# Kernel tuning notes

Hardware: AMD Instinct MI355X
Metric: run time of the kernel (lower is better)

## Reference

```python
import jax, jax.numpy as jnp
import numpy as np

N = 50000      # nodes
E = 800000     # edges (avg degree 16)
EMB = 128      # emb_dim
NF = 7         # x_features
EF = 5         # edge_features
L = 5          # num_layer
BN_EPS = 1e-5


def setup_inputs() -> dict:
    key = jax.random.key(0)
    ks = jax.random.split(key, 12)
    s = 0.05
    return {
        "x": jax.random.normal(ks[0], (N, NF), jnp.float32),
        "edge_attr": jax.random.normal(ks[1], (E, EF), jnp.float32),
        "edge_index": jax.random.randint(ks[2], (2, E), 0, N, dtype=jnp.int32),
        "W_x": jax.random.normal(ks[3], (NF, EMB), jnp.float32) * s,
        "b_x": jax.random.normal(ks[4], (NF, EMB), jnp.float32) * s,
        "W_e": jax.random.normal(ks[5], (L, EF, EMB), jnp.float32) * s,
        "b_e": jax.random.normal(ks[6], (L, EF, EMB), jnp.float32) * s,
        # per-layer GIN update MLP: Linear(EMB,2EMB)-ReLU-Linear(2EMB,EMB)
        "W1": jax.random.normal(ks[7], (L, EMB, 2 * EMB), jnp.float32) * s,
        "b1": jnp.zeros((L, 2 * EMB), jnp.float32),
        "W2": jax.random.normal(ks[8], (L, 2 * EMB, EMB), jnp.float32) * s,
        "b2": jnp.zeros((L, EMB), jnp.float32),
        # per-layer BatchNorm1d affine params
        "gamma": jnp.ones((L, EMB), jnp.float32),
        "beta": jnp.zeros((L, EMB), jnp.float32),
    }


def reference(x, edge_attr, W_x, b_x, W_e, b_e, W1, b1, W2, b2, gamma, beta, edge_index):
    src, dst = edge_index[0], edge_index[1]
    # initial node embedding: sum of 7 Linear(1,EMB) applied per column == x @ W_x + sum(biases)
    h = x @ W_x + b_x.sum(axis=0)  # [N, EMB]
    for l in range(L):
        # edge embeddings: sum of EF Linear(1,EMB) over edge_attr columns
        e_emb = edge_attr @ W_e[l] + b_e[l].sum(axis=0)  # [E, EMB]
        sl_emb = b_e[l].sum(axis=0)  # self-loop edges have zero attr -> bias sum
        # message = x_j + edge_emb, aggr = add (scatter over dst); self loops add h + sl_emb
        msg = h[src] + e_emb                                        # [E, EMB]
        agg = jax.ops.segment_sum(msg, dst, num_segments=N) + h + sl_emb  # [N, EMB]
        # GIN update MLP
        z = jax.nn.relu(agg @ W1[l] + b1[l]) @ W2[l] + b2[l]        # [N, EMB]
        # BatchNorm1d (training-mode batch stats, biased variance)
        mu = z.mean(axis=0)
        var = z.var(axis=0)
        z = (z - mu) * jax.lax.rsqrt(var + BN_EPS) * gamma[l] + beta[l]
        # ELU on all but last layer; dropout is identity at drop_ratio=0; JK='last'
        h = jax.nn.elu(z) if l < L - 1 else z
    return h
```

## Files before the change

### kernel.cpp

```cpp
#include <hip/hip_runtime.h>
#include <math.h>

#define NN 50000
#define NE 800000
#define EMB 128
#define HID 256
#define NF 7
#define EF 5
#define NL 5
#define BN_EPS 1e-5f
#define NREP 32
#define SCAN_B 196
#define NBUCK 49

typedef _Float16 f16x8 __attribute__((ext_vector_type(8)));
typedef _Float16 f16x2 __attribute__((ext_vector_type(2)));
typedef __attribute__((ext_vector_type(4))) float f32x4;

__device__ inline unsigned pkh2(float a, float b) {
    union { unsigned v; _Float16 h[2]; } x;
    x.h[0] = (_Float16)a; x.h[1] = (_Float16)b;
    return x.v;
}
__device__ inline float2 uph2(unsigned u) {
    union { unsigned v; _Float16 h[2]; } x; x.v = u;
    return make_float2((float)x.h[0], (float)x.h[1]);
}
__device__ inline unsigned short f2h_bits(float f) {
    _Float16 h = (_Float16)f;
    return __builtin_bit_cast(unsigned short, h);
}
__device__ inline float h_bits2f(unsigned short b) {
    return (float)__builtin_bit_cast(_Float16, b);
}
__device__ inline f16x2 as_h2(unsigned u) { return __builtin_bit_cast(f16x2, u); }

__global__ void k_prep(const float* __restrict__ b_x, const float* __restrict__ b_e,
                       float* __restrict__ bsum_x, float* __restrict__ bsum_e,
                       int* __restrict__ counts, int* __restrict__ cursor,
                       float* __restrict__ stats) {
    int tid = threadIdx.x;
    if (blockIdx.x == 0 && tid < EMB) {
        float s = 0.f;
        for (int f = 0; f < NF; ++f) s += b_x[f * EMB + tid];
        bsum_x[tid] = s;
        for (int l = 0; l < NL; ++l) {
            float se = 0.f;
            for (int f = 0; f < EF; ++f) se += b_e[(l * EF + f) * EMB + tid];
            bsum_e[l * EMB + tid] = se;
        }
    }
    int gid = blockIdx.x * blockDim.x + tid;
    int stride = gridDim.x * blockDim.x;
    for (int i = gid; i < NN; i += stride) { counts[i] = 0; cursor[i] = 0; }
    const int STOT = NL * NREP * 2 * EMB;
    for (int i = gid; i < STOT; i += stride) stats[i] = 0.f;
}

__global__ void k_prepw(const float* __restrict__ W1, const float* __restrict__ W2,
                        unsigned short* __restrict__ W1ph, unsigned short* __restrict__ W1pl,
                        unsigned short* __restrict__ W2ph, unsigned short* __restrict__ W2pl) {
    const int TOT = NL * EMB * HID;
    int gid = blockIdx.x * blockDim.x + threadIdx.x;
    if (gid < TOT) {
        int l = gid / (EMB * HID);
        int r = gid % (EMB * HID);
        int w = r >> 13;
        int rem = r & 8191;
        int h2 = rem >> 11;
        int rem2 = rem & 2047;
        int kk = rem2 >> 9;
        int rem3 = rem2 & 511;
        int lane = rem3 >> 3;
        int j = rem3 & 7;
        int hc = w * 64 + h2 * 16 + (lane & 15);
        int k = kk * 32 + (lane >> 4) * 8 + j;
        float wv = W1[((size_t)l * EMB + k) * HID + hc];
        unsigned short hi = f2h_bits(wv);
        W1ph[gid] = hi;
        W1pl[gid] = f2h_bits(wv - h_bits2f(hi));
    } else if (gid < 2 * TOT) {
        int g = gid - TOT;
        int l = g / (EMB * HID);
        int r = g % (EMB * HID);
        int w = r >> 13;
        int rem = r & 8191;
        int o2 = rem >> 12;
        int rem2 = rem & 4095;
        int kk = rem2 >> 9;
        int rem3 = rem2 & 511;
        int lane = rem3 >> 3;
        int j = rem3 & 7;
        int oc = w * 32 + o2 * 16 + (lane & 15);
        int k2 = kk * 32 + (lane >> 4) * 8 + j;
        float wv = W2[((size_t)l * HID + k2) * EMB + oc];
        unsigned short hi = f2h_bits(wv);
        W2ph[g] = hi;
        W2pl[g] = f2h_bits(wv - h_bits2f(hi));
    }
}

__global__ void k_init(const float* __restrict__ x, const float* __restrict__ W_x,
                       const float* __restrict__ bsum_x, unsigned short* __restrict__ h16) {
    int gid = blockIdx.x * blockDim.x + threadIdx.x;
    int v = gid >> 5;
    if (v >= NN) return;
    int c = (gid & 31) << 2;
    float4 acc = *(const float4*)(bsum_x + c);
    #pragma unroll
    for (int f = 0; f < NF; ++f) {
        float xv = x[(size_t)v * NF + f];
        float4 w = *(const float4*)(W_x + f * EMB + c);
        acc.x += xv * w.x; acc.y += xv * w.y; acc.z += xv * w.z; acc.w += xv * w.w;
    }
    uint2 p = make_uint2(pkh2(acc.x, acc.y), pkh2(acc.z, acc.w));
    *(uint2*)(h16 + (size_t)v * EMB + c) = p;
}

__global__ void k_hist(const int* __restrict__ dst, int* __restrict__ counts) {
    int e = blockIdx.x * blockDim.x + threadIdx.x;
    if (e < NE) atomicAdd(&counts[dst[e]], 1);
}

__global__ void k_scan1(const int* __restrict__ counts, int* __restrict__ bsum) {
    int tid = threadIdx.x;
    int i = blockIdx.x * 256 + tid;
    int v = (i < NN) ? counts[i] : 0;
    #pragma unroll
    for (int off = 1; off < 64; off <<= 1) v += __shfl_xor(v, off, 64);
    __shared__ int ws[4];
    if ((tid & 63) == 0) ws[tid >> 6] = v;
    __syncthreads();
    if (tid == 0) bsum[blockIdx.x] = ws[0] + ws[1] + ws[2] + ws[3];
}

__global__ void k_scan2(const int* __restrict__ bsum, int* __restrict__ bpre,
                        int* __restrict__ row_start) {
    int tid = threadIdx.x;
    int x = (tid < SCAN_B) ? bsum[tid] : 0;
    int lane = tid & 63, wv = tid >> 6;
    int v = x;
    #pragma unroll
    for (int off = 1; off < 64; off <<= 1) {
        int t = __shfl_up(v, off, 64);
        if (lane >= off) v += t;
    }
    __shared__ int wsum[4];
    if (lane == 63) wsum[wv] = v;
    __syncthreads();
    int woff = 0;
    #pragma unroll
    for (int w = 0; w < 4; ++w) if (w < wv) woff += wsum[w];
    int incl = v + woff;
    if (tid < SCAN_B) bpre[tid] = incl - x;
    if (tid == 255) row_start[NN] = incl;
}

__global__ void k_scan3(const int* __restrict__ counts, const int* __restrict__ bpre,
                        int* __restrict__ row_start, int* __restrict__ bcur) {
    int tid = threadIdx.x;
    int i = blockIdx.x * 256 + tid;
    int x = (i < NN) ? counts[i] : 0;
    int lane = tid & 63, wv = tid >> 6;
    int v = x;
    #pragma unroll
    for (int off = 1; off < 64; off <<= 1) {
        int t = __shfl_up(v, off, 64);
        if (lane >= off) v += t;
    }
    __shared__ int wsum[4];
    if (lane == 63) wsum[wv] = v;
    __syncthreads();
    int woff = 0;
    #pragma unroll
    for (int w = 0; w < 4; ++w) if (w < wv) woff += wsum[w];
    if (i < NN) {
        int rs = bpre[blockIdx.x] + v + woff - x;
        row_start[i] = rs;
        if ((i & 1023) == 0) bcur[i >> 10] = rs;
    }
}

#define BPB 2048
__global__ __launch_bounds__(256) void k_bucket(
        const int* __restrict__ src, const int* __restrict__ dst,
        const float* __restrict__ edge_attr,
        int* __restrict__ bcur, uint4* __restrict__ grouped) {
    __shared__ int lcnt[NBUCK];
    __shared__ int lbase[NBUCK];
    int tid = threadIdx.x;
    if (tid < NBUCK) lcnt[tid] = 0;
    __syncthreads();
    int base = blockIdx.x * BPB;
    int b_[8];
    int d_[8];
    #pragma unroll
    for (int k = 0; k < 8; ++k) {
        int e = base + k * 256 + tid;
        if (e < NE) {
            int d = dst[e];
            d_[k] = d;
            b_[k] = d >> 10;
            atomicAdd(&lcnt[b_[k]], 1);
        } else b_[k] = -1;
    }
    __syncthreads();
    if (tid < NBUCK) {
        lbase[tid] = (lcnt[tid] > 0) ? atomicAdd(&bcur[tid], lcnt[tid]) : 0;
        lcnt[tid] = 0;
    }
    __syncthreads();
    #pragma unroll
    for (int k = 0; k < 8; ++k) {
        int e = base + k * 256 + tid;
        if (e < NE) {
            int b = b_[k];
            int off = lbase[b] + atomicAdd(&lcnt[b], 1);
            const float* ea = edge_attr + (size_t)e * EF;
            uint4 pk;
            pk.x = (unsigned)src[e];
            pk.y = pkh2(ea[0], ea[1]);
            pk.z = pkh2(ea[2], ea[3]);
            pk.w = (unsigned)f2h_bits(ea[4]) | ((unsigned)d_[k] << 16);
            grouped[off] = pk;
        }
    }
}

__global__ void k_place(const uint4* __restrict__ grouped,
                        const int* __restrict__ row_start, int* __restrict__ cursor,
                        uint4* __restrict__ sorted_pk) {
    int e = blockIdx.x * blockDim.x + threadIdx.x;
    if (e >= NE) return;
    uint4 pk = grouped[e];
    int d = (int)(pk.w >> 16);
    int pos = atomicAdd(&cursor[d], 1);
    sorted_pk[row_start[d] + pos] = pk;
}

__global__ void k_esum(const uint4* __restrict__ sorted_pk,
                       const int* __restrict__ row_start,
                       float* __restrict__ attsum, int* __restrict__ sorted_srcc) {
    int v = blockIdx.x * blockDim.x + threadIdx.x;
    if (v >= NN) return;
    int e0 = row_start[v], e1 = row_start[v + 1];
    float s0 = 0.f, s1 = 0.f, s2 = 0.f, s3 = 0.f, s4 = 0.f;
    for (int e = e0; e < e1; ++e) {
        uint4 pk = sorted_pk[e];
        sorted_srcc[e] = (int)pk.x;
        float2 a01 = uph2(pk.y), a23 = uph2(pk.z);
        s0 += a01.x; s1 += a01.y; s2 += a23.x; s3 += a23.y;
        s4 += h_bits2f((unsigned short)(pk.w & 0xffffu));
    }
    float* o = attsum + (size_t)v * 8;
    *(float4*)(o) = make_float4(s0, s1, s2, s3);
    *(float4*)(o + 4) = make_float4(s4, (float)(e1 - e0), 0.f, 0.f);
}

__global__ __launch_bounds__(256) void k_agg(
        const unsigned short* __restrict__ h16, const int* __restrict__ sorted_srcc,
        const float* __restrict__ attsum,
        const float* __restrict__ W_e_l, const float* __restrict__ bsum_e_l,
        const int* __restrict__ row_start,
        unsigned short* __restrict__ agg16) {
    int tid = threadIdx.x;
    int gid = blockIdx.x * 256 + tid;
    int v = gid >> 6;
    if (v >= NN) return;
    int c = (gid & 63) << 1;
    float2 we0 = *(const float2*)(W_e_l + 0 * EMB + c);
    float2 we1 = *(const float2*)(W_e_l + 1 * EMB + c);
    float2 we2 = *(const float2*)(W_e_l + 2 * EMB + c);
    float2 we3 = *(const float2*)(W_e_l + 3 * EMB + c);
    float2 we4 = *(const float2*)(W_e_l + 4 * EMB + c);
    float2 bs = *(const float2*)(bsum_e_l + c);
    float2 hv = uph2(*(const unsigned*)(h16 + (size_t)v * EMB + c));
    const float* at = attsum + (size_t)v * 8;
    float4 a03 = *(const float4*)(at);
    float2 a45 = *(const float2*)(at + 4);
    float ax = hv.x + (a45.y + 1.f) * bs.x
             + a03.x*we0.x + a03.y*we1.x + a03.z*we2.x + a03.w*we3.x + a45.x*we4.x;
    float ay = hv.y + (a45.y + 1.f) * bs.y
             + a03.x*we0.y + a03.y*we1.y + a03.z*we2.y + a03.w*we3.y + a45.x*we4.y;
    int e0 = row_start[v], e1 = row_start[v + 1];
    int e = e0;
    for (; e + 16 <= e1; e += 16) {
        int s0 = __builtin_amdgcn_readfirstlane(sorted_srcc[e + 0]);
        int s1 = __builtin_amdgcn_readfirstlane(sorted_srcc[e + 1]);
        int s2 = __builtin_amdgcn_readfirstlane(sorted_srcc[e + 2]);
        int s3 = __builtin_amdgcn_readfirstlane(sorted_srcc[e + 3]);
        int s4 = __builtin_amdgcn_readfirstlane(sorted_srcc[e + 4]);
        int s5 = __builtin_amdgcn_readfirstlane(sorted_srcc[e + 5]);
        int s6 = __builtin_amdgcn_readfirstlane(sorted_srcc[e + 6]);
        int s7 = __builtin_amdgcn_readfirstlane(sorted_srcc[e + 7]);
        int s8 = __builtin_amdgcn_readfirstlane(sorted_srcc[e + 8]);
        int s9 = __builtin_amdgcn_readfirstlane(sorted_srcc[e + 9]);
        int sa = __builtin_amdgcn_readfirstlane(sorted_srcc[e + 10]);
        int sb = __builtin_amdgcn_readfirstlane(sorted_srcc[e + 11]);
        int sc = __builtin_amdgcn_readfirstlane(sorted_srcc[e + 12]);
        int sd = __builtin_amdgcn_readfirstlane(sorted_srcc[e + 13]);
        int se = __builtin_amdgcn_readfirstlane(sorted_srcc[e + 14]);
        int sf = __builtin_amdgcn_readfirstlane(sorted_srcc[e + 15]);
        unsigned u0 = *(const unsigned*)(h16 + (size_t)s0 * EMB + c);
        unsigned u1 = *(const unsigned*)(h16 + (size_t)s1 * EMB + c);
        unsigned u2 = *(const unsigned*)(h16 + (size_t)s2 * EMB + c);
        unsigned u3 = *(const unsigned*)(h16 + (size_t)s3 * EMB + c);
        unsigned u4 = *(const unsigned*)(h16 + (size_t)s4 * EMB + c);
        unsigned u5 = *(const unsigned*)(h16 + (size_t)s5 * EMB + c);
        unsigned u6 = *(const unsigned*)(h16 + (size_t)s6 * EMB + c);
        unsigned u7 = *(const unsigned*)(h16 + (size_t)s7 * EMB + c);
        unsigned u8 = *(const unsigned*)(h16 + (size_t)s8 * EMB + c);
        unsigned u9 = *(const unsigned*)(h16 + (size_t)s9 * EMB + c);
        unsigned ua = *(const unsigned*)(h16 + (size_t)sa * EMB + c);
        unsigned ub = *(const unsigned*)(h16 + (size_t)sb * EMB + c);
        unsigned uc = *(const unsigned*)(h16 + (size_t)sc * EMB + c);
        unsigned ud = *(const unsigned*)(h16 + (size_t)sd * EMB + c);
        unsigned ue = *(const unsigned*)(h16 + (size_t)se * EMB + c);
        unsigned uf = *(const unsigned*)(h16 + (size_t)sf * EMB + c);
        f16x2 pA = ((as_h2(u0) + as_h2(u1)) + (as_h2(u2) + as_h2(u3)))
                 + ((as_h2(u4) + as_h2(u5)) + (as_h2(u6) + as_h2(u7)));
        f16x2 pB = ((as_h2(u8) + as_h2(u9)) + (as_h2(ua) + as_h2(ub)))
                 + ((as_h2(uc) + as_h2(ud)) + (as_h2(ue) + as_h2(uf)));
        ax += (float)pA.x + (float)pB.x;
        ay += (float)pA.y + (float)pB.y;
    }
    for (; e + 8 <= e1; e += 8) {
        int s0 = __builtin_amdgcn_readfirstlane(sorted_srcc[e + 0]);
        int s1 = __builtin_amdgcn_readfirstlane(sorted_srcc[e + 1]);
        int s2 = __builtin_amdgcn_readfirstlane(sorted_srcc[e + 2]);
        int s3 = __builtin_amdgcn_readfirstlane(sorted_srcc[e + 3]);
        int s4 = __builtin_amdgcn_readfirstlane(sorted_srcc[e + 4]);
        int s5 = __builtin_amdgcn_readfirstlane(sorted_srcc[e + 5]);
        int s6 = __builtin_amdgcn_readfirstlane(sorted_srcc[e + 6]);
        int s7 = __builtin_amdgcn_readfirstlane(sorted_srcc[e + 7]);
        unsigned u0 = *(const unsigned*)(h16 + (size_t)s0 * EMB + c);
        unsigned u1 = *(const unsigned*)(h16 + (size_t)s1 * EMB + c);
        unsigned u2 = *(const unsigned*)(h16 + (size_t)s2 * EMB + c);
        unsigned u3 = *(const unsigned*)(h16 + (size_t)s3 * EMB + c);
        unsigned u4 = *(const unsigned*)(h16 + (size_t)s4 * EMB + c);
        unsigned u5 = *(const unsigned*)(h16 + (size_t)s5 * EMB + c);
        unsigned u6 = *(const unsigned*)(h16 + (size_t)s6 * EMB + c);
        unsigned u7 = *(const unsigned*)(h16 + (size_t)s7 * EMB + c);
        f16x2 p07 = ((as_h2(u0) + as_h2(u1)) + (as_h2(u2) + as_h2(u3)))
                  + ((as_h2(u4) + as_h2(u5)) + (as_h2(u6) + as_h2(u7)));
        ax += (float)p07.x;
        ay += (float)p07.y;
    }
    for (; e < e1; ++e) {
        int s = __builtin_amdgcn_readfirstlane(sorted_srcc[e]);
        float2 hs = uph2(*(const unsigned*)(h16 + (size_t)s * EMB + c));
        ax += hs.x;
        ay += hs.y;
    }
    *(unsigned*)(agg16 + (size_t)v * EMB + c) = pkh2(ax, ay);
}

__global__ __launch_bounds__(256) void k_mlp(
        const unsigned short* __restrict__ agg16,
        const unsigned short* __restrict__ W1ph, const unsigned short* __restrict__ W1pl,
        const float* __restrict__ b1_l,
        const unsigned short* __restrict__ W2ph, const unsigned short* __restrict__ W2pl,
        const float* __restrict__ b2_l,
        unsigned short* __restrict__ z16, float* __restrict__ stats_l) {
    __shared__ unsigned short A16[64][136];
    __shared__ unsigned short Hid16[64][264];
    int tid = threadIdx.x;
    int r0 = blockIdx.x * 64;
    int rep = blockIdx.x & (NREP - 1);
    #pragma unroll
    for (int it = 0; it < 4; ++it) {
        int idx = it * 256 + tid;
        int row = idx >> 4;
        int cb = (idx & 15) * 8;
        int grow = r0 + row;
        uint4 val = make_uint4(0u, 0u, 0u, 0u);
        if (grow < NN) val = *(const uint4*)(agg16 + (size_t)grow * EMB + cb);
        *(uint4*)(&A16[row][cb]) = val;
    }
    __syncthreads();
    int wave = tid >> 6, lane = tid & 63;
    int l16 = lane & 15, quad = lane >> 4;
    {
        f16x8 af[4][4];
        #pragma unroll
        for (int nt = 0; nt < 4; ++nt)
            #pragma unroll
            for (int kk = 0; kk < 4; ++kk)
                af[nt][kk] = *(const f16x8*)(&A16[nt * 16 + l16][kk * 32 + quad * 8]);
        #pragma unroll
        for (int h2 = 0; h2 < 4; ++h2) {
            f16x8 whf[4], wlf[4];
            #pragma unroll
            for (int kk = 0; kk < 4; ++kk) {
                size_t off = ((((size_t)(wave * 4 + h2) * 4) + kk) * 64 + lane) * 8;
                whf[kk] = *(const f16x8*)(W1ph + off);
                wlf[kk] = *(const f16x8*)(W1pl + off);
            }
            float4 bv = *(const float4*)(b1_l + wave * 64 + h2 * 16 + quad * 4);
            f32x4 bias = {bv.x, bv.y, bv.z, bv.w};
            #pragma unroll
            for (int nt = 0; nt < 4; ++nt) {
                f32x4 acc = bias;
                #pragma unroll
                for (int kk = 0; kk < 4; ++kk)
                    acc = __builtin_amdgcn_mfma_f32_16x16x32_f16(whf[kk], af[nt][kk], acc, 0, 0, 0);
                #pragma unroll
                for (int kk = 0; kk < 4; ++kk)
                    acc = __builtin_amdgcn_mfma_f32_16x16x32_f16(wlf[kk], af[nt][kk], acc, 0, 0, 0);
                uint2 p;
                p.x = pkh2(fmaxf(acc[0], 0.f), fmaxf(acc[1], 0.f));
                p.y = pkh2(fmaxf(acc[2], 0.f), fmaxf(acc[3], 0.f));
                int col = wave * 64 + h2 * 16 + quad * 4;
                *(uint2*)(&Hid16[nt * 16 + l16][col]) = p;
            }
        }
    }
    __syncthreads();
    float ss[2][4] = {}, sq[2][4] = {};
    #pragma unroll
    for (int o2 = 0; o2 < 2; ++o2) {
        f16x8 w2h[8], w2l[8];
        #pragma unroll
        for (int kk = 0; kk < 8; ++kk) {
            size_t off = ((((size_t)(wave * 2 + o2) * 8) + kk) * 64 + lane) * 8;
            w2h[kk] = *(const f16x8*)(W2ph + off);
            w2l[kk] = *(const f16x8*)(W2pl + off);
        }
        float4 bv = *(const float4*)(b2_l + wave * 32 + o2 * 16 + quad * 4);
        f32x4 bias = {bv.x, bv.y, bv.z, bv.w};
        #pragma unroll
        for (int nt = 0; nt < 4; ++nt) {
            f16x8 hf[8];
            #pragma unroll
            for (int kk = 0; kk < 8; ++kk)
                hf[kk] = *(const f16x8*)(&Hid16[nt * 16 + l16][kk * 32 + quad * 8]);
            f32x4 acc = bias;
            #pragma unroll
            for (int kk = 0; kk < 8; ++kk)
                acc = __builtin_amdgcn_mfma_f32_16x16x32_f16(w2h[kk], hf[kk], acc, 0, 0, 0);
            #pragma unroll
            for (int kk = 0; kk < 8; ++kk)
                acc = __builtin_amdgcn_mfma_f32_16x16x32_f16(w2l[kk], hf[kk], acc, 0, 0, 0);
            int node = r0 + nt * 16 + l16;
            if (node < NN) {
                uint2 p = make_uint2(pkh2(acc[0], acc[1]), pkh2(acc[2], acc[3]));
                *(uint2*)(z16 + (size_t)node * EMB + wave * 32 + o2 * 16 + quad * 4) = p;
                #pragma unroll
                for (int r = 0; r < 4; ++r) {
                    ss[o2][r] += acc[r];
                    sq[o2][r] += acc[r] * acc[r];
                }
            }
        }
    }
    #pragma unroll
    for (int o2 = 0; o2 < 2; ++o2)
        #pragma unroll
        for (int r = 0; r < 4; ++r) {
            float s = ss[o2][r], q = sq[o2][r];
            #pragma unroll
            for (int m = 1; m < 16; m <<= 1) {
                s += __shfl_xor(s, m, 64);
                q += __shfl_xor(q, m, 64);
            }
            if (l16 == 0) {
                int oc = wave * 32 + o2 * 16 + quad * 4 + r;
                atomicAdd(&stats_l[rep * 2 * EMB + oc], s);
                atomicAdd(&stats_l[rep * 2 * EMB + EMB + oc], q);
            }
        }
}

__global__ void k_bnfused(const float* __restrict__ stats_l,
                          const float* __restrict__ gamma_l, const float* __restrict__ beta_l,
                          const unsigned short* __restrict__ z16,
                          unsigned short* __restrict__ h16, float* __restrict__ fout, int last) {
    __shared__ float red[2 * EMB];
    __shared__ float sc[EMB], sh[EMB];
    int tid = threadIdx.x;
    {
        float acc = 0.f;
        #pragma unroll
        for (int r = 0; r < NREP; ++r) acc += stats_l[r * 2 * EMB + tid];
        red[tid] = acc;
    }
    __syncthreads();
    if (tid < EMB) {
        float s = red[tid], q = red[EMB + tid];
        float mu = s * (1.f / NN);
        float var = q * (1.f / NN) - mu * mu;
        float sf = gamma_l[tid] * rsqrtf(var + BN_EPS);
        sc[tid] = sf;
        sh[tid] = beta_l[tid] - mu * sf;
    }
    __syncthreads();
    const int TOT = NN * EMB / 4;
    for (int gid = blockIdx.x * 256 + tid; gid < TOT; gid += gridDim.x * 256) {
        int c = (gid & 31) << 2;
        uint2 zp = *(const uint2*)(z16 + (size_t)gid * 4);
        float2 z01 = uph2(zp.x), z23 = uph2(zp.y);
        float o0 = z01.x * sc[c + 0] + sh[c + 0];
        float o1 = z01.y * sc[c + 1] + sh[c + 1];
        float o2 = z23.x * sc[c + 2] + sh[c + 2];
        float o3 = z23.y * sc[c + 3] + sh[c + 3];
        if (!last) {
            o0 = (o0 > 0.f) ? o0 : (__expf(o0) - 1.f);
            o1 = (o1 > 0.f) ? o1 : (__expf(o1) - 1.f);
            o2 = (o2 > 0.f) ? o2 : (__expf(o2) - 1.f);
            o3 = (o3 > 0.f) ? o3 : (__expf(o3) - 1.f);
            uint2 p = make_uint2(pkh2(o0, o1), pkh2(o2, o3));
            *(uint2*)(h16 + (size_t)gid * 4) = p;
        } else {
            *(float4*)(fout + (size_t)gid * 4) = make_float4(o0, o1, o2, o3);
        }
    }
}

extern "C" void kernel_launch(void* const* d_in, const int* in_sizes, int n_in,
                              void* d_out, int out_size, void* d_ws, size_t ws_size,
                              hipStream_t stream) {
    const float* x         = (const float*)d_in[0];
    const float* edge_attr = (const float*)d_in[1];
    const int*   edge_idx  = (const int*)d_in[2];
    const float* W_x   = (const float*)d_in[3];
    const float* b_x   = (const float*)d_in[4];
    const float* W_e   = (const float*)d_in[5];
    const float* b_e   = (const float*)d_in[6];
    const float* W1    = (const float*)d_in[7];
    const float* b1    = (const float*)d_in[8];
    const float* W2    = (const float*)d_in[9];
    const float* b2    = (const float*)d_in[10];
    const float* gamma = (const float*)d_in[11];
    const float* beta  = (const float*)d_in[12];
    float* fout = (float*)d_out;

    const int* src = edge_idx;
    const int* dst = edge_idx + NE;

    char* p = (char*)d_ws;
    auto alloc = [&](size_t bytes) { char* q = p; p += (bytes + 255) & ~(size_t)255; return q; };
    unsigned short* h16  = (unsigned short*)alloc((size_t)NN * EMB * 2);
    unsigned short* z16  = (unsigned short*)alloc((size_t)NN * EMB * 2);
    unsigned short* agg16 = (unsigned short*)alloc((size_t)NN * EMB * 2);
    unsigned short* W1ph = (unsigned short*)alloc((size_t)NL * HID * EMB * 2);
    unsigned short* W1pl = (unsigned short*)alloc((size_t)NL * HID * EMB * 2);
    unsigned short* W2ph = (unsigned short*)alloc((size_t)NL * EMB * HID * 2);
    unsigned short* W2pl = (unsigned short*)alloc((size_t)NL * EMB * HID * 2);
    int*   row_start  = (int*)alloc((NN + 1) * sizeof(int));
    int*   counts     = (int*)alloc(NN * sizeof(int));
    int*   cursor     = (int*)alloc(NN * sizeof(int));
    uint4* grouped    = (uint4*)alloc((size_t)NE * sizeof(uint4));
    uint4* sorted_pk  = (uint4*)alloc((size_t)NE * sizeof(uint4));
    int*   sorted_srcc= (int*)alloc((size_t)NE * sizeof(int));
    float* attsum     = (float*)alloc((size_t)NN * 8 * sizeof(float));
    int*   bsum       = (int*)alloc(SCAN_B * sizeof(int));
    int*   bpre       = (int*)alloc(SCAN_B * sizeof(int));
    int*   bcur       = (int*)alloc(NBUCK * sizeof(int));
    float* stats      = (float*)alloc((size_t)NL * NREP * 2 * EMB * sizeof(float));
    float* bsum_x     = (float*)alloc(EMB * sizeof(float));
    float* bsum_e     = (float*)alloc(NL * EMB * sizeof(float));

    k_prep<<<256, 256, 0, stream>>>(b_x, b_e, bsum_x, bsum_e, counts, cursor, stats);
    k_prepw<<<(2 * NL * EMB * HID + 255) / 256, 256, 0, stream>>>(W1, W2, W1ph, W1pl, W2ph, W2pl);
    k_init<<<(NN * 32 + 255) / 256, 256, 0, stream>>>(x, W_x, bsum_x, h16);
    k_hist<<<(NE + 255) / 256, 256, 0, stream>>>(dst, counts);
    k_scan1<<<SCAN_B, 256, 0, stream>>>(counts, bsum);
    k_scan2<<<1, 256, 0, stream>>>(bsum, bpre, row_start);
    k_scan3<<<SCAN_B, 256, 0, stream>>>(counts, bpre, row_start, bcur);
    k_bucket<<<(NE + BPB - 1) / BPB, 256, 0, stream>>>(src, dst, edge_attr, bcur, grouped);
    k_place<<<(NE + 255) / 256, 256, 0, stream>>>(grouped, row_start, cursor, sorted_pk);
    k_esum<<<SCAN_B, 256, 0, stream>>>(sorted_pk, row_start, attsum, sorted_srcc);
    const int AGG_GRID = (NN * 64 + 255) / 256;
    for (int l = 0; l < NL; ++l) {
        float* stats_l = stats + (size_t)l * NREP * 2 * EMB;
        k_agg<<<AGG_GRID, 256, 0, stream>>>(
            h16, sorted_srcc, attsum,
            W_e + (size_t)l * EF * EMB, bsum_e + l * EMB, row_start,
            agg16);
        k_mlp<<<(NN + 63) / 64, 256, 0, stream>>>(
            agg16,
            W1ph + (size_t)l * HID * EMB, W1pl + (size_t)l * HID * EMB, b1 + (size_t)l * HID,
            W2ph + (size_t)l * EMB * HID, W2pl + (size_t)l * EMB * HID, b2 + (size_t)l * EMB,
            z16, stats_l);
        k_bnfused<<<2048, 256, 0, stream>>>(
            stats_l, gamma + l * EMB, beta + l * EMB, z16, h16, fout, (l == NL - 1) ? 1 : 0);
    }
}
```

Baseline: 576.7 us.

## Process two destination nodes per wavefront with predicated batched tail gathers

Each 64-lane wavefront now aggregates two consecutive destination nodes instead of one, halving the aggregation grid. The remainder edges of both nodes (up to 23 each) are loaded through clamped, branch-free index reads and gathers issued together, then accumulated under predicates. The aim is more independent gather loads in flight per wave and fewer serialized tail loops. The cost is higher register pressure, and redundant clamped loads are issued for short rows.

```diff
diff --git a/kernel.cpp b/kernel.cpp
--- a/kernel.cpp
+++ b/kernel.cpp
@@ -257,6 +257,14 @@
     *(float4*)(o + 4) = make_float4(s4, (float)(e1 - e0), 0.f, 0.f);
 }
 
+#define IDXQ(N, k) \
+    int s##N##k = __builtin_amdgcn_readfirstlane( \
+        sorted_srcc[(e##N + k < e1##N) ? (e##N + k) : cb##N]);
+#define GTHQ(N, k) \
+    unsigned u##N##k = *(const unsigned*)(h16 + (size_t)s##N##k * EMB + c);
+#define ACCG(N, k) \
+    if (e##N + k < e1##N) { float2 g = uph2(u##N##k); ax##N += g.x; ay##N += g.y; }
+
 __global__ __launch_bounds__(256) void k_agg(
         const unsigned short* __restrict__ h16, const int* __restrict__ sorted_srcc,
         const float* __restrict__ attsum,
@@ -265,8 +273,10 @@
         unsigned short* __restrict__ agg16) {
     int tid = threadIdx.x;
     int gid = blockIdx.x * 256 + tid;
-    int v = gid >> 6;
-    if (v >= NN) return;
+    int w = gid >> 6;
+    int vA = w << 1;
+    if (vA >= NN) return;
+    int vB = vA + 1;
     int c = (gid & 63) << 1;
     float2 we0 = *(const float2*)(W_e_l + 0 * EMB + c);
     float2 we1 = *(const float2*)(W_e_l + 1 * EMB + c);
@@ -274,85 +284,135 @@
     float2 we3 = *(const float2*)(W_e_l + 3 * EMB + c);
     float2 we4 = *(const float2*)(W_e_l + 4 * EMB + c);
     float2 bs = *(const float2*)(bsum_e_l + c);
-    float2 hv = uph2(*(const unsigned*)(h16 + (size_t)v * EMB + c));
-    const float* at = attsum + (size_t)v * 8;
-    float4 a03 = *(const float4*)(at);
-    float2 a45 = *(const float2*)(at + 4);
-    float ax = hv.x + (a45.y + 1.f) * bs.x
-             + a03.x*we0.x + a03.y*we1.x + a03.z*we2.x + a03.w*we3.x + a45.x*we4.x;
-    float ay = hv.y + (a45.y + 1.f) * bs.y
-             + a03.x*we0.y + a03.y*we1.y + a03.z*we2.y + a03.w*we3.y + a45.x*we4.y;
-    int e0 = row_start[v], e1 = row_start[v + 1];
-    int e = e0;
-    for (; e + 16 <= e1; e += 16) {
-        int s0 = __builtin_amdgcn_readfirstlane(sorted_srcc[e + 0]);
-        int s1 = __builtin_amdgcn_readfirstlane(sorted_srcc[e + 1]);
-        int s2 = __builtin_amdgcn_readfirstlane(sorted_srcc[e + 2]);
-        int s3 = __builtin_amdgcn_readfirstlane(sorted_srcc[e + 3]);
-        int s4 = __builtin_amdgcn_readfirstlane(sorted_srcc[e + 4]);
-        int s5 = __builtin_amdgcn_readfirstlane(sorted_srcc[e + 5]);
-        int s6 = __builtin_amdgcn_readfirstlane(sorted_srcc[e + 6]);
-        int s7 = __builtin_amdgcn_readfirstlane(sorted_srcc[e + 7]);
-        int s8 = __builtin_amdgcn_readfirstlane(sorted_srcc[e + 8]);
-        int s9 = __builtin_amdgcn_readfirstlane(sorted_srcc[e + 9]);
-        int sa = __builtin_amdgcn_readfirstlane(sorted_srcc[e + 10]);
-        int sb = __builtin_amdgcn_readfirstlane(sorted_srcc[e + 11]);
-        int sc = __builtin_amdgcn_readfirstlane(sorted_srcc[e + 12]);
-        int sd = __builtin_amdgcn_readfirstlane(sorted_srcc[e + 13]);
-        int se = __builtin_amdgcn_readfirstlane(sorted_srcc[e + 14]);
-        int sf = __builtin_amdgcn_readfirstlane(sorted_srcc[e + 15]);
-        unsigned u0 = *(const unsigned*)(h16 + (size_t)s0 * EMB + c);
-        unsigned u1 = *(const unsigned*)(h16 + (size_t)s1 * EMB + c);
-        unsigned u2 = *(const unsigned*)(h16 + (size_t)s2 * EMB + c);
-        unsigned u3 = *(const unsigned*)(h16 + (size_t)s3 * EMB + c);
-        unsigned u4 = *(const unsigned*)(h16 + (size_t)s4 * EMB + c);
-        unsigned u5 = *(const unsigned*)(h16 + (size_t)s5 * EMB + c);
-        unsigned u6 = *(const unsigned*)(h16 + (size_t)s6 * EMB + c);
-        unsigned u7 = *(const unsigned*)(h16 + (size_t)s7 * EMB + c);
-        unsigned u8 = *(const unsigned*)(h16 + (size_t)s8 * EMB + c);
-        unsigned u9 = *(const unsigned*)(h16 + (size_t)s9 * EMB + c);
-        unsigned ua = *(const unsigned*)(h16 + (size_t)sa * EMB + c);
-        unsigned ub = *(const unsigned*)(h16 + (size_t)sb * EMB + c);
-        unsigned uc = *(const unsigned*)(h16 + (size_t)sc * EMB + c);
-        unsigned ud = *(const unsigned*)(h16 + (size_t)sd * EMB + c);
-        unsigned ue = *(const unsigned*)(h16 + (size_t)se * EMB + c);
-        unsigned uf = *(const unsigned*)(h16 + (size_t)sf * EMB + c);
-        f16x2 pA = ((as_h2(u0) + as_h2(u1)) + (as_h2(u2) + as_h2(u3)))
-                 + ((as_h2(u4) + as_h2(u5)) + (as_h2(u6) + as_h2(u7)));
-        f16x2 pB = ((as_h2(u8) + as_h2(u9)) + (as_h2(ua) + as_h2(ub)))
-                 + ((as_h2(uc) + as_h2(ud)) + (as_h2(ue) + as_h2(uf)));
-        ax += (float)pA.x + (float)pB.x;
-        ay += (float)pA.y + (float)pB.y;
-    }
-    for (; e + 8 <= e1; e += 8) {
-        int s0 = __builtin_amdgcn_readfirstlane(sorted_srcc[e + 0]);
-        int s1 = __builtin_amdgcn_readfirstlane(sorted_srcc[e + 1]);
-        int s2 = __builtin_amdgcn_readfirstlane(sorted_srcc[e + 2]);
-        int s3 = __builtin_amdgcn_readfirstlane(sorted_srcc[e + 3]);
-        int s4 = __builtin_amdgcn_readfirstlane(sorted_srcc[e + 4]);
-        int s5 = __builtin_amdgcn_readfirstlane(sorted_srcc[e + 5]);
-        int s6 = __builtin_amdgcn_readfirstlane(sorted_srcc[e + 6]);
-        int s7 = __builtin_amdgcn_readfirstlane(sorted_srcc[e + 7]);
-        unsigned u0 = *(const unsigned*)(h16 + (size_t)s0 * EMB + c);
-        unsigned u1 = *(const unsigned*)(h16 + (size_t)s1 * EMB + c);
-        unsigned u2 = *(const unsigned*)(h16 + (size_t)s2 * EMB + c);
-        unsigned u3 = *(const unsigned*)(h16 + (size_t)s3 * EMB + c);
-        unsigned u4 = *(const unsigned*)(h16 + (size_t)s4 * EMB + c);
-        unsigned u5 = *(const unsigned*)(h16 + (size_t)s5 * EMB + c);
-        unsigned u6 = *(const unsigned*)(h16 + (size_t)s6 * EMB + c);
-        unsigned u7 = *(const unsigned*)(h16 + (size_t)s7 * EMB + c);
-        f16x2 p07 = ((as_h2(u0) + as_h2(u1)) + (as_h2(u2) + as_h2(u3)))
-                  + ((as_h2(u4) + as_h2(u5)) + (as_h2(u6) + as_h2(u7)));
-        ax += (float)p07.x;
-        ay += (float)p07.y;
-    }
-    for (; e < e1; ++e) {
-        int s = __builtin_amdgcn_readfirstlane(sorted_srcc[e]);
-        float2 hs = uph2(*(const unsigned*)(h16 + (size_t)s * EMB + c));
-        ax += hs.x;
-        ay += hs.y;
-    }
-    *(unsigned*)(agg16 + (size_t)v * EMB + c) = pkh2(ax, ay);
+    float2 hvA = uph2(*(const unsigned*)(h16 + (size_t)vA * EMB + c));
+    float2 hvB = uph2(*(const unsigned*)(h16 + (size_t)vB * EMB + c));
+    const float* atA = attsum + (size_t)vA * 8;
+    const float* atB = attsum + (size_t)vB * 8;
+    float4 a03A = *(const float4*)(atA);
+    float2 a45A = *(const float2*)(atA + 4);
+    float4 a03B = *(const float4*)(atB);
+    float2 a45B = *(const float2*)(atB + 4);
+    int e0A = row_start[vA];
+    int e1A = row_start[vA + 1];
+    int e1B = row_start[vA + 2];
+    int e0B = e1A;
+    float axA = hvA.x + (a45A.y + 1.f) * bs.x
+              + a03A.x*we0.x + a03A.y*we1.x + a03A.z*we2.x + a03A.w*we3.x + a45A.x*we4.x;
+    float ayA = hvA.y + (a45A.y + 1.f) * bs.y
+              + a03A.x*we0.y + a03A.y*we1.y + a03A.z*we2.y + a03A.w*we3.y + a45A.x*we4.y;
+    float axB = hvB.x + (a45B.y + 1.f) * bs.x
+              + a03B.x*we0.x + a03B.y*we1.x + a03B.z*we2.x + a03B.w*we3.x + a45B.x*we4.x;
+    float ayB = hvB.y + (a45B.y + 1.f) * bs.y
+              + a03B.x*we0.y + a03B.y*we1.y + a03B.z*we2.y + a03B.w*we3.y + a45B.x*we4.y;
+    int eA = e0A, eB = e0B;
+    auto bulk16 = [&](int& e, int e1, float& ax, float& ay) {
+        for (; e + 24 <= e1; e += 16) {
+            int s0 = __builtin_amdgcn_readfirstlane(sorted_srcc[e + 0]);
+            int s1 = __builtin_amdgcn_readfirstlane(sorted_srcc[e + 1]);
+            int s2 = __builtin_amdgcn_readfirstlane(sorted_srcc[e + 2]);
+            int s3 = __builtin_amdgcn_readfirstlane(sorted_srcc[e + 3]);
+            int s4 = __builtin_amdgcn_readfirstlane(sorted_srcc[e + 4]);
+            int s5 = __builtin_amdgcn_readfirstlane(sorted_srcc[e + 5]);
+            int s6 = __builtin_amdgcn_readfirstlane(sorted_srcc[e + 6]);
+            int s7 = __builtin_amdgcn_readfirstlane(sorted_srcc[e + 7]);
+            int s8 = __builtin_amdgcn_readfirstlane(sorted_srcc[e + 8]);
+            int s9 = __builtin_amdgcn_readfirstlane(sorted_srcc[e + 9]);
+            int sa = __builtin_amdgcn_readfirstlane(sorted_srcc[e + 10]);
+            int sb = __builtin_amdgcn_readfirstlane(sorted_srcc[e + 11]);
+            int sc = __builtin_amdgcn_readfirstlane(sorted_srcc[e + 12]);
+            int sd = __builtin_amdgcn_readfirstlane(sorted_srcc[e + 13]);
+            int se = __builtin_amdgcn_readfirstlane(sorted_srcc[e + 14]);
+            int sf = __builtin_amdgcn_readfirstlane(sorted_srcc[e + 15]);
+            unsigned u0 = *(const unsigned*)(h16 + (size_t)s0 * EMB + c);
+            unsigned u1 = *(const unsigned*)(h16 + (size_t)s1 * EMB + c);
+            unsigned u2 = *(const unsigned*)(h16 + (size_t)s2 * EMB + c);
+            unsigned u3 = *(const unsigned*)(h16 + (size_t)s3 * EMB + c);
+            unsigned u4 = *(const unsigned*)(h16 + (size_t)s4 * EMB + c);
+            unsigned u5 = *(const unsigned*)(h16 + (size_t)s5 * EMB + c);
+            unsigned u6 = *(const unsigned*)(h16 + (size_t)s6 * EMB + c);
+            unsigned u7 = *(const unsigned*)(h16 + (size_t)s7 * EMB + c);
+            unsigned u8 = *(const unsigned*)(h16 + (size_t)s8 * EMB + c);
+            unsigned u9 = *(const unsigned*)(h16 + (size_t)s9 * EMB + c);
+            unsigned ua = *(const unsigned*)(h16 + (size_t)sa * EMB + c);
+            unsigned ub = *(const unsigned*)(h16 + (size_t)sb * EMB + c);
+            unsigned uc = *(const unsigned*)(h16 + (size_t)sc * EMB + c);
+            unsigned ud = *(const unsigned*)(h16 + (size_t)sd * EMB + c);
+            unsigned ue = *(const unsigned*)(h16 + (size_t)se * EMB + c);
+            unsigned uf = *(const unsigned*)(h16 + (size_t)sf * EMB + c);
+            f16x2 pA = ((as_h2(u0) + as_h2(u1)) + (as_h2(u2) + as_h2(u3)))
+                     + ((as_h2(u4) + as_h2(u5)) + (as_h2(u6) + as_h2(u7)));
+            f16x2 pB = ((as_h2(u8) + as_h2(u9)) + (as_h2(ua) + as_h2(ub)))
+                     + ((as_h2(uc) + as_h2(ud)) + (as_h2(ue) + as_h2(uf)));
+            ax += (float)pA.x + (float)pB.x;
+            ay += (float)pA.y + (float)pB.y;
+        }
+    };
+    bulk16(eA, e1A, axA, ayA);
+    bulk16(eB, e1B, axB, ayB);
+    int nA = e1A - eA;
+    int nB = e1B - eB;
+    if (nA > 0 || nB > 0) {
+        int cbA = (e1A - 1 >= 0) ? e1A - 1 : 0;
+        int cbB = (e1B - 1 >= 0) ? e1B - 1 : 0;
+        IDXQ(A, 0)  IDXQ(A, 1)  IDXQ(A, 2)  IDXQ(A, 3)  IDXQ(A, 4)  IDXQ(A, 5)
+        IDXQ(A, 6)  IDXQ(A, 7)  IDXQ(A, 8)  IDXQ(A, 9)  IDXQ(A, 10) IDXQ(A, 11)
+        IDXQ(A, 12) IDXQ(A, 13) IDXQ(A, 14) IDXQ(A, 15) IDXQ(A, 16) IDXQ(A, 17)
+        IDXQ(A, 18) IDXQ(A, 19) IDXQ(A, 20) IDXQ(A, 21) IDXQ(A, 22)
+        IDXQ(B, 0)  IDXQ(B, 1)  IDXQ(B, 2)  IDXQ(B, 3)  IDXQ(B, 4)  IDXQ(B, 5)
+        IDXQ(B, 6)  IDXQ(B, 7)  IDXQ(B, 8)  IDXQ(B, 9)  IDXQ(B, 10) IDXQ(B, 11)
+        IDXQ(B, 12) IDXQ(B, 13) IDXQ(B, 14) IDXQ(B, 15) IDXQ(B, 16) IDXQ(B, 17)
+        IDXQ(B, 18) IDXQ(B, 19) IDXQ(B, 20) IDXQ(B, 21) IDXQ(B, 22)
+        GTHQ(A, 0)  GTHQ(A, 1)  GTHQ(A, 2)  GTHQ(A, 3)  GTHQ(A, 4)  GTHQ(A, 5)
+        GTHQ(A, 6)  GTHQ(A, 7)  GTHQ(A, 8)  GTHQ(A, 9)  GTHQ(A, 10) GTHQ(A, 11)
+        GTHQ(A, 12) GTHQ(A, 13) GTHQ(A, 14) GTHQ(A, 15) GTHQ(A, 16) GTHQ(A, 17)
+        GTHQ(A, 18) GTHQ(A, 19) GTHQ(A, 20) GTHQ(A, 21) GTHQ(A, 22)
+        GTHQ(B, 0)  GTHQ(B, 1)  GTHQ(B, 2)  GTHQ(B, 3)  GTHQ(B, 4)  GTHQ(B, 5)
+        GTHQ(B, 6)  GTHQ(B, 7)  GTHQ(B, 8)  GTHQ(B, 9)  GTHQ(B, 10) GTHQ(B, 11)
+        GTHQ(B, 12) GTHQ(B, 13) GTHQ(B, 14) GTHQ(B, 15) GTHQ(B, 16) GTHQ(B, 17)
+        GTHQ(B, 18) GTHQ(B, 19) GTHQ(B, 20) GTHQ(B, 21) GTHQ(B, 22)
+        if (nA >= 16) {
+            f16x2 pA = ((as_h2(uA0) + as_h2(uA1)) + (as_h2(uA2) + as_h2(uA3)))
+                     + ((as_h2(uA4) + as_h2(uA5)) + (as_h2(uA6) + as_h2(uA7)));
+            f16x2 pB2 = ((as_h2(uA8) + as_h2(uA9)) + (as_h2(uA10) + as_h2(uA11)))
+                      + ((as_h2(uA12) + as_h2(uA13)) + (as_h2(uA14) + as_h2(uA15)));
+            axA += (float)pA.x + (float)pB2.x;
+            ayA += (float)pA.y + (float)pB2.y;
+            ACCG(A, 16) ACCG(A, 17) ACCG(A, 18) ACCG(A, 19)
+            ACCG(A, 20) ACCG(A, 21) ACCG(A, 22)
+        } else if (nA >= 8) {
+            f16x2 p07 = ((as_h2(uA0) + as_h2(uA1)) + (as_h2(uA2) + as_h2(uA3)))
+                      + ((as_h2(uA4) + as_h2(uA5)) + (as_h2(uA6) + as_h2(uA7)));
+            axA += (float)p07.x;
+            ayA += (float)p07.y;
+            ACCG(A, 8)  ACCG(A, 9)  ACCG(A, 10) ACCG(A, 11)
+            ACCG(A, 12) ACCG(A, 13) ACCG(A, 14)
+        } else if (nA >= 1) {
+            ACCG(A, 0) ACCG(A, 1) ACCG(A, 2) ACCG(A, 3)
+            ACCG(A, 4) ACCG(A, 5) ACCG(A, 6)
+        }
+        if (nB >= 16) {
+            f16x2 pA = ((as_h2(uB0) + as_h2(uB1)) + (as_h2(uB2) + as_h2(uB3)))
+                     + ((as_h2(uB4) + as_h2(uB5)) + (as_h2(uB6) + as_h2(uB7)));
+            f16x2 pB2 = ((as_h2(uB8) + as_h2(uB9)) + (as_h2(uB10) + as_h2(uB11)))
+                      + ((as_h2(uB12) + as_h2(uB13)) + (as_h2(uB14) + as_h2(uB15)));
+            axB += (float)pA.x + (float)pB2.x;
+            ayB += (float)pA.y + (float)pB2.y;
+            ACCG(B, 16) ACCG(B, 17) ACCG(B, 18) ACCG(B, 19)
+            ACCG(B, 20) ACCG(B, 21) ACCG(B, 22)
+        } else if (nB >= 8) {
+            f16x2 p07 = ((as_h2(uB0) + as_h2(uB1)) + (as_h2(uB2) + as_h2(uB3)))
+                      + ((as_h2(uB4) + as_h2(uB5)) + (as_h2(uB6) + as_h2(uB7)));
+            axB += (float)p07.x;
+            ayB += (float)p07.y;
+            ACCG(B, 8)  ACCG(B, 9)  ACCG(B, 10) ACCG(B, 11)
+            ACCG(B, 12) ACCG(B, 13) ACCG(B, 14)
+        } else if (nB >= 1) {
+            ACCG(B, 0) ACCG(B, 1) ACCG(B, 2) ACCG(B, 3)
+            ACCG(B, 4) ACCG(B, 5) ACCG(B, 6)
+        }
+    }
+    *(unsigned*)(agg16 + (size_t)vA * EMB + c) = pkh2(axA, ayA);
+    *(unsigned*)(agg16 + (size_t)vB * EMB + c) = pkh2(axB, ayB);
 }
 
 __global__ __launch_bounds__(256) void k_mlp(
@@ -570,7 +630,7 @@
     k_bucket<<<(NE + BPB - 1) / BPB, 256, 0, stream>>>(src, dst, edge_attr, bcur, grouped);
     k_place<<<(NE + 255) / 256, 256, 0, stream>>>(grouped, row_start, cursor, sorted_pk);
     k_esum<<<SCAN_B, 256, 0, stream>>>(sorted_pk, row_start, attsum, sorted_srcc);
-    const int AGG_GRID = (NN * 64 + 255) / 256;
+    const int AGG_GRID = ((NN / 2) * 64 + 255) / 256;
     for (int l = 0; l < NL; ++l) {
         float* stats_l = stats + (size_t)l * NREP * 2 * EMB;
         k_agg<<<AGG_GRID, 256, 0, stream>>>(
```

Result: faster. 538.2 us (-6.7%).
